# Optimization experiments

Measured on AMD Instinct MI355X. Metric: run time of the kernel, lower is better.

The kernel has to match this reference:

```python
import jax, jax.numpy as jnp
import numpy as np

D = 64        # d_model
HEADS = 4
DH = D // HEADS   # 16 per-head dim (shared QK)
DEPTH = 4
NHASH = 4
BS = 64       # bucket_size
FF = 4 * D
SELF_ATTN_VAL = -5e4  # reformer-pytorch TOKEN_SELF_ATTN_VALUE


def layer_norm(x, g, b, eps=1e-5):
    m = x.mean(-1, keepdims=True)
    v = ((x - m) ** 2).mean(-1, keepdims=True)
    return (x - m) * jax.lax.rsqrt(v + eps) * g + b


def lsh_attention(x, wqk, wv, wo_w, wo_b, rot):
    # x: (B, L, D); rot: (DH, NHASH, n_buckets//2) fixed random rotations
    B, L, _ = x.shape
    nb = L // BS                       # n_buckets
    qk = x @ wqk                        # shared query/key projection, no bias
    v = x @ wv

    def split_heads(t):
        return t.reshape(B, L, HEADS, DH).transpose(0, 2, 1, 3).reshape(B * HEADS, L, DH)

    qk, v = split_heads(qk), split_heads(v)
    Bh = B * HEADS

    # --- LSH hashing: argmax over [rot, -rot] projections ---
    rotated = jnp.einsum('btf,fhi->bhti', qk, rot)          # (Bh, NHASH, L, nb//2)
    rotated = jnp.concatenate([rotated, -rotated], axis=-1)  # (Bh, NHASH, L, nb)
    buckets = jnp.argmax(rotated, axis=-1)                   # (Bh, NHASH, L)
    offsets = (jnp.arange(NHASH) * nb)[None, :, None]
    buckets = (buckets + offsets).reshape(Bh, NHASH * L)

    # --- sort tokens by (bucket, position) ---
    ticker = jnp.arange(NHASH * L)
    bkt_t = buckets * L + (ticker % L)[None, :]
    sticker = jnp.argsort(bkt_t, axis=-1)
    undo_sort = jnp.argsort(sticker, axis=-1)
    st = sticker % L                                          # (Bh, NHASH*L)

    sqk = jnp.take_along_axis(qk, st[..., None], axis=1)
    sv = jnp.take_along_axis(v, st[..., None], axis=1)

    n_chunks = NHASH * nb
    bq_t = st.reshape(Bh, n_chunks, BS)
    bqk = sqk.reshape(Bh, n_chunks, BS, DH)
    bv = sv.reshape(Bh, n_chunks, BS, DH)
    bq = bqk
    bk = bqk / jnp.maximum(jnp.linalg.norm(bqk, axis=-1, keepdims=True), 1e-12)

    def look_one_back(t):
        return jnp.concatenate([t, jnp.roll(t, 1, axis=1)], axis=2)

    bk = look_one_back(bk)                    # (Bh, n_chunks, 2*BS, DH)
    bv = look_one_back(bv)
    bkv_t = look_one_back(bq_t[..., None])[..., 0]  # (Bh, n_chunks, 2*BS)

    dots = jnp.einsum('bcie,bcje->bcij', bq, bk) * (DH ** -0.5)
    self_mask = bq_t[:, :, :, None] == bkv_t[:, :, None, :]
    dots = jnp.where(self_mask, SELF_ATTN_VAL, dots)

    lse = jax.scipy.special.logsumexp(dots, axis=-1, keepdims=True)
    probs = jnp.exp(dots - lse)
    bo = jnp.einsum('bcij,bcje->bcie', probs, bv)

    so = bo.reshape(Bh, NHASH * L, DH)
    slog = lse.reshape(Bh, NHASH * L)
    o = jnp.take_along_axis(so, undo_sort[..., None], axis=1).reshape(Bh, NHASH, L, DH)
    logits = jnp.take_along_axis(slog, undo_sort, axis=1).reshape(Bh, NHASH, L, 1)

    # combine hash rounds weighted by their softmax normalizers
    w = jnp.exp(logits - jax.scipy.special.logsumexp(logits, axis=1, keepdims=True))
    out = (o * w).sum(axis=1)                 # (Bh, L, DH)
    out = out.reshape(B, HEADS, L, DH).transpose(0, 2, 1, 3).reshape(B, L, D)
    return out @ wo_w + wo_b


def feed_forward(x, w1, b1, w2, b2):
    return jax.nn.gelu(x @ w1 + b1, approximate=False) @ w2 + b2


def setup_inputs() -> dict:
    key = jax.random.key(0)
    ks = jax.random.split(key, 12)
    B = 16
    s = 0.02
    nb = 1280 // BS  # 20 buckets at padded seq len
    return {
        'wave': jax.random.normal(ks[0], (B, 2, 1250), jnp.float32),
        'in_w': jax.random.normal(ks[1], (2, D), jnp.float32) * s,
        'in_b': jnp.zeros((D,), jnp.float32),
        'ln1_g': jnp.ones((DEPTH, D), jnp.float32),
        'ln1_b': jnp.zeros((DEPTH, D), jnp.float32),
        'wqk': jax.random.normal(ks[2], (DEPTH, D, D), jnp.float32) * s,
        'wv': jax.random.normal(ks[3], (DEPTH, D, D), jnp.float32) * s,
        'wo_w': jax.random.normal(ks[4], (DEPTH, D, D), jnp.float32) * s,
        'wo_b': jnp.zeros((DEPTH, D), jnp.float32),
        'rot': jax.random.normal(ks[5], (DEPTH, DH, NHASH, nb // 2), jnp.float32),
        'ln2_g': jnp.ones((DEPTH, D), jnp.float32),
        'ln2_b': jnp.zeros((DEPTH, D), jnp.float32),
        'w1': jax.random.normal(ks[6], (DEPTH, D, FF), jnp.float32) * s,
        'b1': jnp.zeros((DEPTH, FF), jnp.float32),
        'w2': jax.random.normal(ks[7], (DEPTH, FF, D), jnp.float32) * s,
        'b2': jnp.zeros((DEPTH, D), jnp.float32),
        'out_w': jax.random.normal(ks[8], (D, 1), jnp.float32) * s,
        'out_b': jnp.zeros((1,), jnp.float32),
    }


def reference(wave, in_w, in_b, ln1_g, ln1_b, wqk, wv, wo_w, wo_b, rot,
              ln2_g, ln2_b, w1, b1, w2, b2, out_w, out_b):
    x = wave.transpose(0, 2, 1)               # (B, 1250, 2)
    L0 = x.shape[1]
    pad = (-L0) % (BS * 2)                    # pad to multiple of 128 -> 1280
    x = jnp.pad(x, ((0, 0), (0, pad), (0, 0)))
    x = x @ in_w + in_b                       # (B, L, D)

    # reversible sequence: y1 = x1 + attn(LN(x2)); y2 = x2 + ff(LN(y1))
    x1 = x2 = x
    for i in range(DEPTH):
        x1 = x1 + lsh_attention(layer_norm(x2, ln1_g[i], ln1_b[i]),
                                wqk[i], wv[i], wo_w[i], wo_b[i], rot[i])
        x2 = x2 + feed_forward(layer_norm(x1, ln2_g[i], ln2_b[i]),
                               w1[i], b1[i], w2[i], b2[i])
    x = (x1 + x2) * 0.5
    y = (x @ out_w + out_b)[..., 0]
    return y[:, :L0]
```

## Files before the change

kernel.cpp:

```cpp
#include <hip/hip_runtime.h>
#include <math.h>

#define LSEQ 1280
#define L0SEQ 1250
#define DM 64
#define NHEADS 4
#define DHD 16
#define NHASH 4
#define NBUK 20
#define NCHUNK 80
#define FFD 256
#define NBATCH 16
#define NBH 64

#define XSZ (NBATCH*LSEQ*DM)
#define QKSZ (NBH*LSEQ*DHD)
#define OHSZ (NBH*NHASH*LSEQ*DHD)
#define SLSZ (NBH*NHASH*LSEQ)

typedef __attribute__((ext_vector_type(8))) short frag_ab;
typedef __attribute__((ext_vector_type(4))) float frag_c;

union FU4 { uint4 v; frag_ab f; };

__device__ __forceinline__ unsigned rnbf(float x){
    unsigned b = __float_as_uint(x);
    return (b + 0x7fffu + ((b >> 16) & 1u)) >> 16;
}
__device__ __forceinline__ float bf2f(unsigned h){ return __uint_as_float(h << 16); }
__device__ __forceinline__ unsigned rot16(unsigned x){ return (x >> 16) | (x << 16); }
__device__ __forceinline__ uint4 rot16v(uint4 a){
    uint4 r; r.x=rot16(a.x); r.y=rot16(a.y); r.z=rot16(a.z); r.w=rot16(a.w); return r;
}

__device__ __forceinline__ void split3(float x, unsigned& h, unsigned& m, unsigned& l){
    unsigned bx = __float_as_uint(x);
    h = bx >> 16;
    float r = x - __uint_as_float(bx & 0xffff0000u);
    unsigned br = __float_as_uint(r);
    m = br >> 16;
    float r2 = r - __uint_as_float(br & 0xffff0000u);
    l = __float_as_uint(r2) >> 16;
}

__device__ __forceinline__ unsigned pack_hm(float x){
    unsigned bx = __float_as_uint(x);
    float r = x - __uint_as_float(bx & 0xffff0000u);
    return __builtin_amdgcn_perm(__float_as_uint(r), bx, 0x07060302u);
}

__device__ __forceinline__ unsigned pack_hm_rn(float x){
    unsigned h = rnbf(x);
    unsigned m = rnbf(x - bf2f(h));
    return h | (m << 16);
}

__device__ __forceinline__ void split_hml(float x, unsigned& hm, unsigned& l){
    unsigned bx = __float_as_uint(x);
    float r = x - __uint_as_float(bx & 0xffff0000u);
    unsigned br = __float_as_uint(r);
    hm = __builtin_amdgcn_perm(br, bx, 0x07060302u);
    float r2 = r - __uint_as_float(br & 0xffff0000u);
    l = __float_as_uint(r2) >> 16;
}

__device__ __forceinline__ float gelu_fast(float x){
    float ax = fabsf(x) * 0.70710678118654752f;
    float t = __builtin_amdgcn_rcpf(1.f + 0.3275911f*ax);
    float poly = ((((1.061405429f*t - 1.453152027f)*t + 1.421413741f)*t
                   - 0.284496736f)*t + 0.254829592f)*t;
    float e = 1.f - poly * __expf(-ax*ax);
    float er = __uint_as_float((__float_as_uint(e) & 0x7fffffffu) |
                               (__float_as_uint(x) & 0x80000000u));
    return 0.5f*x*(1.f + er);
}

__global__ __launch_bounds__(256) void k_init(
    const float* __restrict__ wave, const float* __restrict__ in_w, const float* __restrict__ in_b,
    float* __restrict__ x1, float* __restrict__ x2,
    const float* __restrict__ wo_w, const float* __restrict__ w1,
    const float* __restrict__ w2, unsigned* __restrict__ wsplit)
{
    if (blockIdx.x < 5120) {
        int idx = blockIdx.x * 256 + threadIdx.x;
        int d = idx & 63;
        int t = idx >> 6;
        int b = t / LSEQ;
        int tt = t % LSEQ;
        float v0 = 0.f, v1 = 0.f;
        if (tt < L0SEQ) {
            v0 = wave[(size_t)(b*2+0)*L0SEQ + tt];
            v1 = wave[(size_t)(b*2+1)*L0SEQ + tt];
        }
        float x = v0 * in_w[d] + v1 * in_w[64 + d] + in_b[d];
        x1[idx] = x;
        x2[idx] = x;
    } else {
        int gid = (blockIdx.x - 5120) * 256 + threadIdx.x;
        int l = gid / 36864;
        int r = gid % 36864;
        float src; unsigned* dst; int idx; int stride;
        if (r < 4096) {
            int k = r >> 6, n = r & 63;
            src = wo_w[l*4096 + k*64 + n];
            dst = wsplit + l*8192;
            idx = (((k>>4)*4 + (n>>4))*16 + (n&15))*16 + (k&15);
            stride = 4096;
        } else if (r < 20480) {
            int rr = r - 4096;
            int k = rr >> 8, n = rr & 255;
            src = w1[l*16384 + k*256 + n];
            dst = wsplit + 32768 + l*32768;
            idx = (((k>>4)*16 + (n>>4))*16 + (n&15))*16 + (k&15);
            stride = 16384;
        } else {
            int rr = r - 20480;
            int k = rr >> 6, n = rr & 63;
            src = w2[l*16384 + k*64 + n];
            dst = wsplit + 163840 + l*32768;
            idx = (((k>>4)*4 + (n>>4))*16 + (n&15))*16 + (k&15);
            stride = 16384;
        }
        unsigned h, m, lo;
        split3(src, h, m, lo);
        dst[idx]          = h | (m<<16);
        dst[idx + stride] = lo | (h<<16);
    }
}

__global__ __launch_bounds__(256) void k_qkv(
    const float* __restrict__ x2, const float* __restrict__ g, const float* __restrict__ bta,
    const float* __restrict__ wqk, const float* __restrict__ wv, const float* __restrict__ rot,
    unsigned* __restrict__ qkvs, int* __restrict__ buckets)
{
    __shared__ float xln[16][68];
    __shared__ float qkt[16][68];
    __shared__ float vvt[16][68];
    __shared__ float rots[640];
    int tid = threadIdx.x;
    int b  = blockIdx.x / 80;
    int t0 = (blockIdx.x % 80) * 16;
    int tok = tid >> 4;
    int cg  = tid & 15;
    int c4  = cg * 4;

    for (int i = tid; i < 640; i += 256) rots[i] = rot[i];

    float4 xv4 = *(const float4*)&x2[((size_t)b*LSEQ + t0 + tok)*DM + c4];
    float s = xv4.x + xv4.y + xv4.z + xv4.w;
    float ss = xv4.x*xv4.x + xv4.y*xv4.y + xv4.z*xv4.z + xv4.w*xv4.w;
    s  += __shfl_xor(s,1);  s  += __shfl_xor(s,2);  s  += __shfl_xor(s,4);  s  += __shfl_xor(s,8);
    ss += __shfl_xor(ss,1); ss += __shfl_xor(ss,2); ss += __shfl_xor(ss,4); ss += __shfl_xor(ss,8);
    float m = s * (1.f/64.f);
    float vr = ss * (1.f/64.f) - m*m;
    float rstd = 1.f / sqrtf(vr + 1e-5f);
    {
        float4 g4 = *(const float4*)&g[c4];
        float4 b4 = *(const float4*)&bta[c4];
        float4 o;
        o.x = (xv4.x-m)*rstd*g4.x + b4.x;
        o.y = (xv4.y-m)*rstd*g4.y + b4.y;
        o.z = (xv4.z-m)*rstd*g4.z + b4.z;
        o.w = (xv4.w-m)*rstd*g4.w + b4.w;
        *(float4*)&xln[tok][c4] = o;
    }
    __syncthreads();

    float aq[4] = {0,0,0,0}, av[4] = {0,0,0,0};
    for (int f = 0; f < 64; f++) {
        float4 wq4 = *(const float4*)&wqk[f*64 + c4];
        float4 wv4 = *(const float4*)&wv [f*64 + c4];
        float xv = xln[tok][f];
        aq[0] += xv*wq4.x; aq[1] += xv*wq4.y; aq[2] += xv*wq4.z; aq[3] += xv*wq4.w;
        av[0] += xv*wv4.x; av[1] += xv*wv4.y; av[2] += xv*wv4.z; av[3] += xv*wv4.w;
    }
    *(float4*)&qkt[tok][c4] = *(float4*)aq;
    *(float4*)&vvt[tok][c4] = *(float4*)av;
    __syncthreads();

    int p = tid >> 2;
    int ptok = p >> 2, head = p & 3;
    int sub = tid & 3;
    int e0 = sub * 4;
    int t = t0 + ptok;
    float4 qf4 = *(const float4*)&qkt[ptok][head*16 + e0];
    float nsq = qf4.x*qf4.x + qf4.y*qf4.y + qf4.z*qf4.z + qf4.w*qf4.w;
    nsq += __shfl_xor(nsq,1); nsq += __shfl_xor(nsq,2);
    float inv = 1.f / fmaxf(sqrtf(nsq), 1e-12f);
    float qe[4] = {qf4.x, qf4.y, qf4.z, qf4.w};
    unsigned wq[4], wk[4];
    #pragma unroll
    for (int i=0;i<4;i++){
        float xq = qe[i]*0.25f;
        unsigned qh = rnbf(xq);
        unsigned ql = rnbf(xq - bf2f(qh));
        wq[i] = qh | (ql<<16);
        float xk = qe[i]*inv;
        unsigned kh = rnbf(xk);
        unsigned kl = rnbf(xk - bf2f(kh));
        wk[i] = kh | (kl<<16);
    }
    float4 vf4 = *(const float4*)&vvt[ptok][head*16 + e0];
    unsigned wv1[4];
    wv1[0] = pack_hm_rn(vf4.x); wv1[1] = pack_hm_rn(vf4.y);
    wv1[2] = pack_hm_rn(vf4.z); wv1[3] = pack_hm_rn(vf4.w);
    size_t sb = (((size_t)(b*NHEADS+head))*LSEQ + t)*64;
    *(uint4*)&qkvs[sb + e0]      = *(uint4*)wq;
    *(uint4*)&qkvs[sb + 16 + e0] = *(uint4*)wk;
    *(uint4*)&qkvs[sb + 32 + e0] = *(uint4*)wv1;

    float qf[16];
    {
        float4 a0 = *(const float4*)&qkt[ptok][head*16 + 0];
        float4 a1 = *(const float4*)&qkt[ptok][head*16 + 4];
        float4 a2 = *(const float4*)&qkt[ptok][head*16 + 8];
        float4 a3 = *(const float4*)&qkt[ptok][head*16 + 12];
        qf[0]=a0.x; qf[1]=a0.y; qf[2]=a0.z; qf[3]=a0.w;
        qf[4]=a1.x; qf[5]=a1.y; qf[6]=a1.z; qf[7]=a1.w;
        qf[8]=a2.x; qf[9]=a2.y; qf[10]=a2.z; qf[11]=a2.w;
        qf[12]=a3.x; qf[13]=a3.y; qf[14]=a3.z; qf[15]=a3.w;
    }
    int nh = sub;
    float rv[10];
    #pragma unroll
    for (int i=0;i<10;i++) {
        float acc = 0.f;
        #pragma unroll
        for (int f=0; f<16; f++) acc += qf[f]*rots[(f*NHASH+nh)*10 + i];
        rv[i] = acc;
    }
    float best = rv[0]; int bi = 0;
    #pragma unroll
    for (int i=1;i<10;i++) if (rv[i] > best) { best = rv[i]; bi = i; }
    #pragma unroll
    for (int i=0;i<10;i++) if (-rv[i] > best) { best = -rv[i]; bi = 10+i; }
    buckets[((size_t)(b*NHEADS+head)*NHASH + nh)*LSEQ + t] = bi;
}

__global__ __launch_bounds__(256) void k_sort(
    const int* __restrict__ buckets, int* __restrict__ sorted)
{
    __shared__ unsigned long long masks[20][20];
    __shared__ int pre[20][20];
    __shared__ int startl[20];
    int tid = threadIdx.x;
    int w = tid >> 6, lane = tid & 63;
    int gidx = blockIdx.x;
    const int* bk = buckets + (size_t)gidx * LSEQ;
    int* dst = sorted + (size_t)gidx * LSEQ;

    int myb[5];
    #pragma unroll
    for (int i = 0; i < 5; i++) {
        int ch = w*5 + i;
        int bv = bk[ch*64 + lane];
        myb[i] = bv;
        #pragma unroll
        for (int b2 = 0; b2 < 20; b2++) {
            unsigned long long m2 = __ballot(bv == b2);
            if (lane == b2) masks[ch][b2] = m2;
        }
    }
    __syncthreads();
    if (tid < 20) {
        int run = 0;
        for (int ch = 0; ch < 20; ch++) {
            pre[ch][tid] = run;
            run += __popcll(masks[ch][tid]);
        }
        startl[tid] = run;
    }
    __syncthreads();
    if (tid == 0) {
        int acc = 0;
        for (int b2 = 0; b2 < 20; b2++) { int t = startl[b2]; startl[b2] = acc; acc += t; }
    }
    __syncthreads();
    unsigned long long below = (lane == 63) ? 0x7fffffffffffffffull
                                            : ((1ull << lane) - 1ull);
    #pragma unroll
    for (int i = 0; i < 5; i++) {
        int ch = w*5 + i;
        int bv = myb[i];
        int rank = startl[bv] + pre[ch][bv] + __popcll(masks[ch][bv] & below);
        dst[rank] = ch*64 + lane;
    }
}

__global__ __launch_bounds__(256) void k_attn(
    const unsigned* __restrict__ qkvs,
    const int* __restrict__ sorted, float* __restrict__ o_hash, float* __restrict__ slog)
{
    __shared__ __align__(16) unsigned SM[5312];
    unsigned* Va1 = SM;
    unsigned* Ka1 = SM + 2624;
    unsigned* Pa1 = SM + 2624;
    int* kposS = (int*)(SM + 5184);

    int tid = threadIdx.x;
    int bh = blockIdx.x & 63;
    int c  = blockIdx.x >> 6;
    int h  = c / NBUK, cc = c % NBUK;
    int cp = (c + NCHUNK - 1) % NCHUNK;
    int hp = cp / NBUK, ccp = cp % NBUK;

    int key = tid & 127;
    int pos = (key < 64)
        ? sorted[((size_t)bh*NHASH + h)*LSEQ + cc*64 + key]
        : sorted[((size_t)bh*NHASH + hp)*LSEQ + ccp*64 + (key-64)];
    size_t srow = ((size_t)bh*LSEQ + pos)*64;
    if (tid < 128) {
        kposS[key] = pos;
        const uint4* kr = (const uint4*)(qkvs + srow + 16);
        #pragma unroll
        for (int e4=0; e4<4; e4++)
            *(uint4*)&Ka1[key*20 + e4*4] = kr[e4];
    } else {
        const uint4* v1r = (const uint4*)(qkvs + srow + 32);
        int kt = key >> 4, jl = key & 15;
        int lb = kt*328 + jl;
        #pragma unroll
        for (int e4=0; e4<4; e4++){
            uint4 a = v1r[e4];
            unsigned aa[4] = {a.x,a.y,a.z,a.w};
            #pragma unroll
            for (int i=0;i<4;i++){
                int d = e4*4 + i;
                Va1[lb + d*20] = aa[i];
            }
        }
    }
    __syncthreads();

    int w = tid >> 6, lane = tid & 63;
    int quad = lane >> 4, col = lane & 15;

    int qgpos = kposS[16*w + col];
    FU4 QA;
    QA.v = *(const uint4*)(qkvs + ((size_t)bh*LSEQ + qgpos)*64 + quad*4);
    frag_ab qA = QA.f;

    frag_c acc[8];
    #pragma unroll
    for (int nt=0; nt<8; nt++){
        FU4 B1, B2;
        B1.v = *(const uint4*)&Ka1[(nt*16+col)*20 + 4*quad];
        B2.v = rot16v(B1.v);
        frag_c a = {0.f,0.f,0.f,0.f};
        a = __builtin_amdgcn_mfma_f32_16x16x32_bf16(qA, B1.f, a, 0, 0, 0);
        a = __builtin_amdgcn_mfma_f32_16x16x32_bf16(qA, B2.f, a, 0, 0, 0);
        acc[nt] = a;
    }
    int qp[4];
    #pragma unroll
    for (int reg=0; reg<4; reg++) qp[reg] = kposS[16*w + quad*4 + reg];

    #pragma unroll
    for (int nt=0; nt<8; nt++) if (nt == w) {
        #pragma unroll
        for (int reg=0; reg<4; reg++)
            acc[nt][reg] = (col == quad*4 + reg) ? -5e4f : acc[nt][reg];
    }
    if (cc == 0) {
        #pragma unroll
        for (int nt=4; nt<8; nt++){
            int kp2 = kposS[nt*16 + col];
            #pragma unroll
            for (int reg=0; reg<4; reg++)
                if (kp2 == qp[reg]) acc[nt][reg] = -5e4f;
        }
    }

    float mx[4] = {-3.4e38f,-3.4e38f,-3.4e38f,-3.4e38f};
    #pragma unroll
    for (int nt=0; nt<8; nt++)
        #pragma unroll
        for (int reg=0; reg<4; reg++) mx[reg] = fmaxf(mx[reg], acc[nt][reg]);
    #pragma unroll
    for (int reg=0; reg<4; reg++){
        float m2 = mx[reg];
        m2 = fmaxf(m2, __shfl_xor(m2, 1)); m2 = fmaxf(m2, __shfl_xor(m2, 2));
        m2 = fmaxf(m2, __shfl_xor(m2, 4)); m2 = fmaxf(m2, __shfl_xor(m2, 8));
        mx[reg] = m2;
    }
    float sm2[4] = {0.f,0.f,0.f,0.f};
    #pragma unroll
    for (int nt=0; nt<8; nt++)
        #pragma unroll
        for (int reg=0; reg<4; reg++){
            float e = __expf(acc[nt][reg] - mx[reg]);
            acc[nt][reg] = e; sm2[reg] += e;
        }
    #pragma unroll
    for (int reg=0; reg<4; reg++){
        float s2 = sm2[reg];
        s2 += __shfl_xor(s2, 1); s2 += __shfl_xor(s2, 2);
        s2 += __shfl_xor(s2, 4); s2 += __shfl_xor(s2, 8);
        sm2[reg] = s2;
    }
    float invs[4];
    #pragma unroll
    for (int reg=0; reg<4; reg++) invs[reg] = __builtin_amdgcn_rcpf(sm2[reg]);
    if (col == 0) {
        #pragma unroll
        for (int reg=0; reg<4; reg++)
            slog[((size_t)bh*NHASH + h)*LSEQ + qp[reg]] = mx[reg] + __logf(sm2[reg]);
    }

    frag_c o = {0.f,0.f,0.f,0.f};
    __syncthreads();
    #pragma unroll
    for (int pass=0; pass<4; pass++){
        #pragma unroll
        for (int t2=0; t2<2; t2++){
            int nt = pass*2 + t2;
            #pragma unroll
            for (int reg=0; reg<4; reg++){
                int idx = t2*1280 + (16*w + 4*quad + reg)*20 + col;
                Pa1[idx] = pack_hm(acc[nt][reg]);
            }
        }
        __syncthreads();
        #pragma unroll
        for (int t2=0; t2<2; t2++){
            int ktg = pass*2 + t2;
            FU4 A1, B1, B2;
            int pidx = t2*1280 + (16*w + col)*20 + 4*quad;
            A1.v = *(const uint4*)&Pa1[pidx];
            int vidx = ktg*328 + col*20 + 4*quad;
            B1.v = *(const uint4*)&Va1[vidx];
            B2.v = rot16v(B1.v);
            o = __builtin_amdgcn_mfma_f32_16x16x32_bf16(A1.f, B1.f, o, 0, 0, 0);
            o = __builtin_amdgcn_mfma_f32_16x16x32_bf16(A1.f, B2.f, o, 0, 0, 0);
        }
        if (pass < 3) __syncthreads();
    }
    size_t obase = ((size_t)bh*NHASH + h)*LSEQ;
    #pragma unroll
    for (int reg=0; reg<4; reg++)
        o_hash[(obase + qp[reg])*DHD + col] = o[reg] * invs[reg];
}

__global__ __launch_bounds__(256) void k_tail(
    const float* __restrict__ o_hash, const float* __restrict__ slog,
    const unsigned* __restrict__ wo_s, const float* __restrict__ wo_b,
    const float* __restrict__ g2, const float* __restrict__ b2t,
    const unsigned* __restrict__ w1_s, const float* __restrict__ b1,
    const unsigned* __restrict__ w2_s, const float* __restrict__ b2f,
    float* __restrict__ x1, float* __restrict__ x2,
    const float* __restrict__ out_w, const float* __restrict__ out_b,
    float* __restrict__ y, int do_out)
{
    __shared__ unsigned cA1[1024];
    __shared__ unsigned short cA2h[1024];
    __shared__ unsigned gA1[4096];
    __shared__ unsigned short gA2h[4096];
    __shared__ float lnS[64], lnQ[64];
    float* red = (float*)gA1;

    int tid = threadIdx.x;
    int b  = blockIdx.x / 80;
    int t0 = (blockIdx.x % 80) * 16;
    int w = tid >> 6, lane = tid & 63;
    int quad = lane >> 4, col = lane & 15;
    int cg = w*16 + col;

    float x1pre[4], x2pre[4];
    #pragma unroll
    for (int reg=0; reg<4; reg++){
        size_t xi = ((size_t)b*LSEQ + t0 + quad*4 + reg)*DM + cg;
        x1pre[reg] = x1[xi];
        x2pre[reg] = x2[xi];
    }
    float wb_pre  = wo_b[cg];
    float gv_pre  = g2[cg];
    float bv_pre  = b2t[cg];
    float bbf_pre = b2f[cg];
    float ow_pre  = out_w[cg];
    float b1v[4];
    #pragma unroll
    for (int ntl=0; ntl<4; ntl++) b1v[ntl] = b1[(w*4 + ntl)*16 + col];

    {
        int tok = tid >> 4;
        int dg  = tid & 15;
        int d0  = dg * 4;
        int kt  = dg >> 2;
        int t = t0 + tok;
        int bh = b*NHEADS + kt;
        float sl[4];
        #pragma unroll
        for (int nh=0; nh<4; nh++) sl[nh] = slog[((size_t)bh*NHASH + nh)*LSEQ + t];
        float mx = fmaxf(fmaxf(sl[0],sl[1]), fmaxf(sl[2],sl[3]));
        float wgt[4]; float wsum = 0.f;
        #pragma unroll
        for (int nh=0; nh<4; nh++){ wgt[nh] = __expf(sl[nh]-mx); wsum += wgt[nh]; }
        float iv = 1.f/wsum;
        float a4[4] = {0.f,0.f,0.f,0.f};
        #pragma unroll
        for (int nh=0; nh<4; nh++){
            float4 oh = *(const float4*)&o_hash[(((size_t)bh*NHASH + nh)*LSEQ + t)*DHD + (d0 & 15)];
            float wn = wgt[nh]*iv;
            a4[0] += wn*oh.x; a4[1] += wn*oh.y; a4[2] += wn*oh.z; a4[3] += wn*oh.w;
        }
        int sw = (tok & 7) << 2;
        unsigned cw1[4], lw[4];
        #pragma unroll
        for (int i=0;i<4;i++) split_hml(a4[i], cw1[i], lw[i]);
        *(uint4*)&cA1[tok*64 + (d0 ^ sw)] = *(uint4*)cw1;
        uint2 lp;
        lp.x = lw[0] | (lw[1]<<16);
        lp.y = lw[2] | (lw[3]<<16);
        *(uint2*)&cA2h[tok*64 + (d0 ^ sw)] = lp;
    }
    __syncthreads();
    FU4 aA1[4], aA2[4];
    {
        int sw = (col & 7) << 2;
        #pragma unroll
        for (int kt=0; kt<4; kt++){
            int word = (kt*16 + quad*4) ^ sw;
            aA1[kt].v = *(const uint4*)&cA1[col*64 + word];
            uint2 zl = *(const uint2*)&cA2h[col*64 + word];
            aA2[kt].v.x = __builtin_amdgcn_perm(zl.x, aA1[kt].v.x, 0x05040100u);
            aA2[kt].v.y = __builtin_amdgcn_perm(zl.x, aA1[kt].v.y, 0x07060100u);
            aA2[kt].v.z = __builtin_amdgcn_perm(zl.y, aA1[kt].v.z, 0x05040100u);
            aA2[kt].v.w = __builtin_amdgcn_perm(zl.y, aA1[kt].v.w, 0x07060100u);
        }
    }

    frag_c awo = {0.f,0.f,0.f,0.f};
    #pragma unroll
    for (int kt=0; kt<4; kt++){
        FU4 B1, B2, B3;
        int bidx = ((kt*4 + w)*16 + col)*16 + quad*4;
        B1.v = *(const uint4*)&wo_s[bidx];
        B2.v = rot16v(B1.v);
        B3.v = *(const uint4*)&wo_s[bidx + 4096];
        awo = __builtin_amdgcn_mfma_f32_16x16x32_bf16(aA1[kt].f, B1.f, awo, 0, 0, 0);
        awo = __builtin_amdgcn_mfma_f32_16x16x32_bf16(aA1[kt].f, B2.f, awo, 0, 0, 0);
        awo = __builtin_amdgcn_mfma_f32_16x16x32_bf16(aA2[kt].f, B3.f, awo, 0, 0, 0);
    }
    float x1n[4];
    float s1[4], s2[4];
    {
        #pragma unroll
        for (int reg=0; reg<4; reg++){
            int rg = t0 + quad*4 + reg;
            size_t xi = ((size_t)b*LSEQ + rg)*DM + cg;
            float xv = x1pre[reg] + awo[reg] + wb_pre;
            x1[xi] = xv;
            x1n[reg] = xv;
            s1[reg] = xv; s2[reg] = xv*xv;
        }
    }
    #pragma unroll
    for (int reg=0; reg<4; reg++){
        float a = s1[reg], q = s2[reg];
        a += __shfl_xor(a,1); a += __shfl_xor(a,2); a += __shfl_xor(a,4); a += __shfl_xor(a,8);
        q += __shfl_xor(q,1); q += __shfl_xor(q,2); q += __shfl_xor(q,4); q += __shfl_xor(q,8);
        s1[reg] = a; s2[reg] = q;
    }
    if (col == 0) {
        #pragma unroll
        for (int reg=0; reg<4; reg++){
            lnS[w*16 + quad*4 + reg] = s1[reg];
            lnQ[w*16 + quad*4 + reg] = s2[reg];
        }
    }
    __syncthreads();
    float mean[4], rstd[4];
    #pragma unroll
    for (int reg=0; reg<4; reg++){
        int tok = quad*4 + reg;
        float a = lnS[tok] + lnS[16+tok] + lnS[32+tok] + lnS[48+tok];
        float q = lnQ[tok] + lnQ[16+tok] + lnQ[32+tok] + lnQ[48+tok];
        mean[reg] = a*(1.f/64.f);
        float var = q*(1.f/64.f) - mean[reg]*mean[reg];
        rstd[reg] = 1.f/sqrtf(var + 1e-5f);
    }
    {
        #pragma unroll
        for (int reg=0; reg<4; reg++){
            int row = quad*4 + reg;
            float xv = (x1n[reg]-mean[reg])*rstd[reg]*gv_pre + bv_pre;
            unsigned hm_, l_;
            split_hml(xv, hm_, l_);
            int word = cg ^ ((row & 7) << 2);
            cA1[row*64 + word] = hm_;
            cA2h[row*64 + word] = (unsigned short)l_;
        }
    }
    __syncthreads();
    FU4 xa1[4], xa2[4];
    {
        int sw = (col & 7) << 2;
        #pragma unroll
        for (int kt=0; kt<4; kt++){
            int word = (kt*16 + quad*4) ^ sw;
            xa1[kt].v = *(const uint4*)&cA1[col*64 + word];
            uint2 zl = *(const uint2*)&cA2h[col*64 + word];
            xa2[kt].v.x = __builtin_amdgcn_perm(zl.x, xa1[kt].v.x, 0x05040100u);
            xa2[kt].v.y = __builtin_amdgcn_perm(zl.x, xa1[kt].v.y, 0x07060100u);
            xa2[kt].v.z = __builtin_amdgcn_perm(zl.y, xa1[kt].v.z, 0x05040100u);
            xa2[kt].v.w = __builtin_amdgcn_perm(zl.y, xa1[kt].v.w, 0x07060100u);
        }
    }

    unsigned* myg1 = gA1 + w*1024;
    unsigned short* myg2h = gA2h + w*1024;
    #pragma unroll
    for (int ntl=0; ntl<4; ntl++){
        int nt = w*4 + ntl;
        frag_c a = {0.f,0.f,0.f,0.f};
        #pragma unroll
        for (int kt=0; kt<4; kt++){
            FU4 B1, B2, B3;
            int bidx = ((kt*16 + nt)*16 + col)*16 + quad*4;
            B1.v = *(const uint4*)&w1_s[bidx];
            B2.v = rot16v(B1.v);
            B3.v = *(const uint4*)&w1_s[bidx + 16384];
            a = __builtin_amdgcn_mfma_f32_16x16x32_bf16(xa1[kt].f, B1.f, a, 0, 0, 0);
            a = __builtin_amdgcn_mfma_f32_16x16x32_bf16(xa1[kt].f, B2.f, a, 0, 0, 0);
            a = __builtin_amdgcn_mfma_f32_16x16x32_bf16(xa2[kt].f, B3.f, a, 0, 0, 0);
        }
        float bb = b1v[ntl];
        #pragma unroll
        for (int reg=0; reg<4; reg++){
            float xx = a[reg] + bb;
            float ge = gelu_fast(xx);
            unsigned hm_, l_;
            split_hml(ge, hm_, l_);
            int row = quad*4 + reg;
            int word = (ntl*16 + col) ^ ((row & 7) << 2);
            myg1[row*64 + word] = hm_;
            myg2h[row*64 + word] = (unsigned short)l_;
        }
    }
    frag_c aw2[4] = {{0,0,0,0},{0,0,0,0},{0,0,0,0},{0,0,0,0}};
    {
        int sw = (col & 7) << 2;
        #pragma unroll
        for (int kt2=0; kt2<4; kt2++){
            FU4 A1, A2;
            int word = (kt2*16 + quad*4) ^ sw;
            A1.v = *(const uint4*)&myg1[col*64 + word];
            uint2 zl = *(const uint2*)&myg2h[col*64 + word];
            A2.v.x = __builtin_amdgcn_perm(zl.x, A1.v.x, 0x05040100u);
            A2.v.y = __builtin_amdgcn_perm(zl.x, A1.v.y, 0x07060100u);
            A2.v.z = __builtin_amdgcn_perm(zl.y, A1.v.z, 0x05040100u);
            A2.v.w = __builtin_amdgcn_perm(zl.y, A1.v.w, 0x07060100u);
            int kg = w*4 + kt2;
            #pragma unroll
            for (int nt2=0; nt2<4; nt2++){
                FU4 B1, B2, B3;
                int bidx = ((kg*4 + nt2)*16 + col)*16 + quad*4;
                B1.v = *(const uint4*)&w2_s[bidx];
                B2.v = rot16v(B1.v);
                B3.v = *(const uint4*)&w2_s[bidx + 16384];
                aw2[nt2] = __builtin_amdgcn_mfma_f32_16x16x32_bf16(A1.f, B1.f, aw2[nt2], 0, 0, 0);
                aw2[nt2] = __builtin_amdgcn_mfma_f32_16x16x32_bf16(A1.f, B2.f, aw2[nt2], 0, 0, 0);
                aw2[nt2] = __builtin_amdgcn_mfma_f32_16x16x32_bf16(A2.f, B3.f, aw2[nt2], 0, 0, 0);
            }
        }
    }
    __syncthreads();
    #pragma unroll
    for (int nt2=0; nt2<4; nt2++)
        #pragma unroll
        for (int reg=0; reg<4; reg++)
            red[((w*4 + nt2)*4 + reg)*64 + lane] = aw2[nt2][reg];
    __syncthreads();
    float x2f[4];
    {
        #pragma unroll
        for (int reg=0; reg<4; reg++){
            float v = red[((0*4 + w)*4 + reg)*64 + lane]
                    + red[((1*4 + w)*4 + reg)*64 + lane]
                    + red[((2*4 + w)*4 + reg)*64 + lane]
                    + red[((3*4 + w)*4 + reg)*64 + lane];
            int rg = t0 + quad*4 + reg;
            size_t xi = ((size_t)b*LSEQ + rg)*DM + cg;
            float nv = x2pre[reg] + v + bbf_pre;
            x2[xi] = nv;
            x2f[reg] = nv;
        }
    }
    if (do_out) {
        float part[4];
        #pragma unroll
        for (int reg=0; reg<4; reg++){
            float p = (x1n[reg] + x2f[reg]) * 0.5f * ow_pre;
            p += __shfl_xor(p,1); p += __shfl_xor(p,2); p += __shfl_xor(p,4); p += __shfl_xor(p,8);
            part[reg] = p;
        }
        __syncthreads();
        if (col == 0) {
            #pragma unroll
            for (int reg=0; reg<4; reg++)
                lnS[w*16 + quad*4 + reg] = part[reg];
        }
        __syncthreads();
        if (tid < 16) {
            int t = t0 + tid;
            if (t < L0SEQ) {
                float v2 = lnS[tid] + lnS[16+tid] + lnS[32+tid] + lnS[48+tid];
                y[(size_t)b*L0SEQ + t] = v2 + out_b[0];
            }
        }
    }
}

extern "C" void kernel_launch(void* const* d_in, const int* in_sizes, int n_in,
                              void* d_out, int out_size, void* d_ws, size_t ws_size,
                              hipStream_t stream)
{
    const float* wave  = (const float*)d_in[0];
    const float* in_w  = (const float*)d_in[1];
    const float* in_b  = (const float*)d_in[2];
    const float* ln1_g = (const float*)d_in[3];
    const float* ln1_b = (const float*)d_in[4];
    const float* wqk   = (const float*)d_in[5];
    const float* wv    = (const float*)d_in[6];
    const float* wo_w  = (const float*)d_in[7];
    const float* wo_b  = (const float*)d_in[8];
    const float* rot   = (const float*)d_in[9];
    const float* ln2_g = (const float*)d_in[10];
    const float* ln2_b = (const float*)d_in[11];
    const float* w1    = (const float*)d_in[12];
    const float* b1    = (const float*)d_in[13];
    const float* w2    = (const float*)d_in[14];
    const float* b2    = (const float*)d_in[15];
    const float* out_w = (const float*)d_in[16];
    const float* out_b = (const float*)d_in[17];
    float* y = (float*)d_out;

    float* ws = (float*)d_ws;
    float* x1      = ws;
    float* x2      = x1 + XSZ;
    unsigned* qkvs = (unsigned*)(x2 + XSZ);
    float* o_hash  = (float*)(qkvs + 4*QKSZ);
    float* slogb   = o_hash + OHSZ;
    int* buckets   = (int*)(slogb + SLSZ);
    int* sorted    = buckets + SLSZ;
    unsigned* wsplit = (unsigned*)(sorted + SLSZ);

    k_init<<<5696, 256, 0, stream>>>(wave, in_w, in_b, x1, x2, wo_w, w1, w2, wsplit);
    for (int layer = 0; layer < 4; layer++) {
        k_qkv<<<NBATCH*80, 256, 0, stream>>>(x2, ln1_g + layer*64, ln1_b + layer*64,
                                       wqk + layer*4096, wv + layer*4096, rot + layer*640,
                                       qkvs, buckets);
        k_sort<<<256, 256, 0, stream>>>(buckets, sorted);
        k_attn<<<NBH*NCHUNK, 256, 0, stream>>>(qkvs, sorted, o_hash, slogb);
        k_tail<<<NBATCH*LSEQ/16, 256, 0, stream>>>(o_hash, slogb,
                                        wsplit + layer*8192, wo_b + layer*64,
                                        ln2_g + layer*64, ln2_b + layer*64,
                                        wsplit + 32768 + layer*32768, b1 + layer*256,
                                        wsplit + 163840 + layer*32768, b2 + layer*64,
                                        x1, x2,
                                        out_w, out_b, y, (layer == 3) ? 1 : 0);
    }
}
```

Baseline: 472.6 us.

## Split FF2 GEMM by output columns per wave instead of K-split reduction

```diff
diff --git a/kernel.cpp b/kernel.cpp
--- a/kernel.cpp
+++ b/kernel.cpp
@@ -456,7 +456,6 @@
     __shared__ unsigned gA1[4096];
     __shared__ unsigned short gA2h[4096];
     __shared__ float lnS[64], lnQ[64];
-    float* red = (float*)gA1;
 
     int tid = threadIdx.x;
     int b  = blockIdx.x / 80;
@@ -637,51 +636,37 @@
             myg2h[row*64 + word] = (unsigned short)l_;
         }
     }
-    frag_c aw2[4] = {{0,0,0,0},{0,0,0,0},{0,0,0,0},{0,0,0,0}};
+    __syncthreads();
+    frag_c aw2 = {0.f,0.f,0.f,0.f};
     {
         int sw = (col & 7) << 2;
         #pragma unroll
-        for (int kt2=0; kt2<4; kt2++){
+        for (int kg=0; kg<16; kg++){
             FU4 A1, A2;
-            int word = (kt2*16 + quad*4) ^ sw;
-            A1.v = *(const uint4*)&myg1[col*64 + word];
-            uint2 zl = *(const uint2*)&myg2h[col*64 + word];
+            int base = (kg>>2)*1024 + col*64 + ((((kg&3)*16) + quad*4) ^ sw);
+            A1.v = *(const uint4*)&gA1[base];
+            uint2 zl = *(const uint2*)&gA2h[base];
             A2.v.x = __builtin_amdgcn_perm(zl.x, A1.v.x, 0x05040100u);
             A2.v.y = __builtin_amdgcn_perm(zl.x, A1.v.y, 0x07060100u);
             A2.v.z = __builtin_amdgcn_perm(zl.y, A1.v.z, 0x05040100u);
             A2.v.w = __builtin_amdgcn_perm(zl.y, A1.v.w, 0x07060100u);
-            int kg = w*4 + kt2;
-            #pragma unroll
-            for (int nt2=0; nt2<4; nt2++){
-                FU4 B1, B2, B3;
-                int bidx = ((kg*4 + nt2)*16 + col)*16 + quad*4;
-                B1.v = *(const uint4*)&w2_s[bidx];
-                B2.v = rot16v(B1.v);
-                B3.v = *(const uint4*)&w2_s[bidx + 16384];
-                aw2[nt2] = __builtin_amdgcn_mfma_f32_16x16x32_bf16(A1.f, B1.f, aw2[nt2], 0, 0, 0);
-                aw2[nt2] = __builtin_amdgcn_mfma_f32_16x16x32_bf16(A1.f, B2.f, aw2[nt2], 0, 0, 0);
-                aw2[nt2] = __builtin_amdgcn_mfma_f32_16x16x32_bf16(A2.f, B3.f, aw2[nt2], 0, 0, 0);
-            }
-        }
-    }
-    __syncthreads();
-    #pragma unroll
-    for (int nt2=0; nt2<4; nt2++)
-        #pragma unroll
-        for (int reg=0; reg<4; reg++)
-            red[((w*4 + nt2)*4 + reg)*64 + lane] = aw2[nt2][reg];
-    __syncthreads();
+            FU4 B1, B2, B3;
+            int bidx = ((kg*4 + w)*16 + col)*16 + quad*4;
+            B1.v = *(const uint4*)&w2_s[bidx];
+            B2.v = rot16v(B1.v);
+            B3.v = *(const uint4*)&w2_s[bidx + 16384];
+            aw2 = __builtin_amdgcn_mfma_f32_16x16x32_bf16(A1.f, B1.f, aw2, 0, 0, 0);
+            aw2 = __builtin_amdgcn_mfma_f32_16x16x32_bf16(A1.f, B2.f, aw2, 0, 0, 0);
+            aw2 = __builtin_amdgcn_mfma_f32_16x16x32_bf16(A2.f, B3.f, aw2, 0, 0, 0);
+        }
+    }
     float x2f[4];
     {
         #pragma unroll
         for (int reg=0; reg<4; reg++){
-            float v = red[((0*4 + w)*4 + reg)*64 + lane]
-                    + red[((1*4 + w)*4 + reg)*64 + lane]
-                    + red[((2*4 + w)*4 + reg)*64 + lane]
-                    + red[((3*4 + w)*4 + reg)*64 + lane];
             int rg = t0 + quad*4 + reg;
             size_t xi = ((size_t)b*LSEQ + rg)*DM + cg;
-            float nv = x2pre[reg] + v + bbf_pre;
+            float nv = x2pre[reg] + aw2[reg] + bbf_pre;
             x2[xi] = nv;
             x2f[reg] = nv;
         }
```

Measured after the change: 483.6 us. +2.3%, slower.
